# Kernel tuning notes

Measured on AMD Instinct MI355X. Metric: run time of the kernel, lower is better.

The kernel has to match this reference:

```python
import jax, jax.numpy as jnp
import numpy as np

EPS = 1e-9
TOP_K = 2


def setup_inputs() -> dict:
    key = jax.random.key(0)
    k = jax.random.split(key, 6)
    B, E, D_IN, D_MODEL, D_SEL = 16384, 8, 900, 512, 128
    return {
        "cycle_curve_data": jax.random.normal(k[0], (B, D_IN), jnp.float32),
        "logits": jax.random.normal(k[1], (B, E), jnp.float32),
        "moe_masks": jax.random.randint(k[2], (B, E), 0, 2, jnp.int32),
        "selection_embeddings": jax.random.normal(k[3], (B, E, D_SEL), jnp.float32),
        "W": jax.random.normal(k[4], (E, D_IN, D_MODEL), jnp.float32) / np.sqrt(D_IN).astype(np.float32),
        "b": jnp.zeros((E, D_MODEL), jnp.float32),
    }


def reference(cycle_curve_data, logits, moe_masks, selection_embeddings, W, b):
    B, E = logits.shape
    mask = (moe_masks == 1).astype(logits.dtype)  # [B, E]
    raw = jax.nn.softmax(logits, axis=1)          # [B, E]

    # inactive-expert mixture for selection embedding
    inactive = raw * (1.0 - mask)
    inactive = inactive / (jnp.sum(inactive, axis=1, keepdims=True) + EPS)
    selection_embedding = jnp.einsum("bes,be->bs", selection_embeddings, inactive)

    # active gates + top-k selection + renormalization
    active = raw * mask
    _, idx = jax.lax.top_k(active, TOP_K)                                  # [B, K]
    top_mask = jnp.sum(jax.nn.one_hot(idx, E, dtype=active.dtype), axis=1)  # [B, E]
    gates = active * top_mask
    gates = gates / (jnp.sum(gates, axis=1, keepdims=True) + EPS)

    # dense formulation of dispatch -> per-expert Linear -> weighted combine:
    # out[b] = sum_e gates[b,e] * (x[b] @ W[e] + b[e])
    expert_out = jnp.einsum("bd,edm->bem", cycle_curve_data, W) + b  # [B, E, D_model]
    final_out = jnp.einsum("bem,be->bm", expert_out, gates).astype(jnp.bfloat16)

    # guide loss (training-mode auxiliary loss)
    s = jnp.sum(raw * mask) / B
    guide_loss = (1.0 - s) * (1.0 - s)
    return final_out, guide_loss, selection_embedding
```

## Files before the change

kernel.cpp:

```cpp
#include <hip/hip_runtime.h>
#include <hip/hip_bf16.h>


#define B_ROWS 16384
#define DIN 900
#define DM 512
#define DSEL 128
#define KP 928
#define NKS 29
#define MAXT 192
#define EPSF 1e-9f

#define OUT_GUIDE (B_ROWS*DM)
#define OUT_SEL   (B_ROWS*DM + 1)

#define WS_COUNTS 0
#define WS_PART   512
#define WS_NT     768
#define WS_OFF    1024
#define WS_ENT    2048
#define WS_BB     9216
#define WS_PIDLR  25600
#define WS_GATEB  91136
#define WS_W8     222208
#define WS_ROWSS  746496
#define WS_WT     812032

typedef __attribute__((ext_vector_type(8))) short short8;
typedef __attribute__((ext_vector_type(8))) unsigned short ushort8;
typedef __attribute__((ext_vector_type(4))) float floatx4;

__device__ inline unsigned short f2bf(float v){
  union { __hip_bfloat16 h; unsigned short u; } c;
  c.h = __float2bfloat16(v);
  return c.u;
}
__device__ inline float bf2f(unsigned short u){
  union { unsigned int i; float f; } c;
  c.i = ((unsigned int)u) << 16;
  return c.f;
}

__global__ __launch_bounds__(256) void cvtw_k(const float* __restrict__ W,
                                              unsigned short* __restrict__ wt){
  __shared__ unsigned short tl[64][65];
  int kt = blockIdx.x, ntb = blockIdx.y, e = blockIdx.z;
  int c = threadIdx.x & 63, q = threadIdx.x >> 6;
  for (int i = 0; i < 16; i++){
    int kl = q + i*4;
    int k = kt*64 + kl;
    float v = (k < DIN) ? W[((size_t)e*DIN + k)*DM + ntb*64 + c] : 0.f;
    tl[kl][c] = f2bf(v);
  }
  __syncthreads();
  for (int i = 0; i < 16; i++){
    int nl = q + i*4;
    int k = kt*64 + c;
    if (k < KP)
      wt[((size_t)e*DM + ntb*64 + nl)*KP + k] = tl[c][nl];
  }
}

__global__ __launch_bounds__(256) void gating_k(const float* __restrict__ logits,
                                                const int* __restrict__ masks,
                                                int* __restrict__ counts,
                                                float* __restrict__ partials,
                                                int* __restrict__ pidlr,
                                                float2* __restrict__ gatesb,
                                                float* __restrict__ w8,
                                                int* __restrict__ blockbase){
  __shared__ int hist[64];
  __shared__ float wsum[4];
  int t = threadIdx.x;
  if (t < 64) hist[t] = 0;
  __syncthreads();
  int b = blockIdx.x*256 + t;
  float4 l0 = *(const float4*)&logits[(size_t)b*8];
  float4 l1 = *(const float4*)&logits[(size_t)b*8 + 4];
  int4  m0 = *(const int4*)&masks[(size_t)b*8];
  int4  m1 = *(const int4*)&masks[(size_t)b*8 + 4];
  float raw[8] = {l0.x,l0.y,l0.z,l0.w,l1.x,l1.y,l1.z,l1.w};
  int   mk[8]  = {m0.x,m0.y,m0.z,m0.w,m1.x,m1.y,m1.z,m1.w};
  float mx = raw[0];
  for (int e = 1; e < 8; e++) mx = fmaxf(mx, raw[e]);
  float Z = 0.f;
  for (int e = 0; e < 8; e++){ raw[e] = expf(raw[e]-mx); Z += raw[e]; }
  float invZ = 1.f/Z;
  float act[8], ina[8]; float srm = 0.f, isum = 0.f;
  for (int e = 0; e < 8; e++){
    raw[e] *= invZ;
    if (mk[e] == 1){ act[e] = raw[e]; ina[e] = 0.f; srm += raw[e]; }
    else           { act[e] = 0.f;    ina[e] = raw[e]; isum += raw[e]; }
  }
  float v1 = -1.f, v2 = -1.f; int e1 = 0, e2 = 0;
  for (int e = 0; e < 8; e++){
    float a = act[e];
    if (a > v1){ v2 = v1; e2 = e1; v1 = a; e1 = e; }
    else if (a > v2){ v2 = a; e2 = e; }
  }
  float den = v1 + v2 + EPSF;
  float g1 = v1/den, g2 = v2/den;
  int lo, hi; float gl, gh;
  if (e1 < e2){ lo = e1; hi = e2; gl = g1; gh = g2; }
  else        { lo = e2; hi = e1; gl = g2; gh = g1; }
  int pid = lo*8 + hi;
  float invI = 1.f/(isum + EPSF);
  for (int e = 0; e < 8; e++) w8[(size_t)b*8 + e] = ina[e]*invI;
  gatesb[b] = make_float2(gl, gh);
  int lr = atomicAdd(&hist[pid], 1);
  pidlr[b] = pid | (lr << 8);
  float s = srm;
  for (int sft = 32; sft > 0; sft >>= 1) s += __shfl_down(s, sft, 64);
  if ((t & 63) == 0) wsum[t >> 6] = s;
  __syncthreads();
  if (t < 64){
    int c = hist[t];
    int base = 0;
    if (c > 0) base = atomicAdd(&counts[t], c);
    blockbase[blockIdx.x*64 + t] = base;
  }
  if (t == 0) partials[blockIdx.x] = wsum[0] + wsum[1] + wsum[2] + wsum[3];
}

__global__ __launch_bounds__(256) void selemb_k(const float* __restrict__ sel,
                                                const float* __restrict__ w8,
                                                const int* __restrict__ pidlr,
                                                const int* __restrict__ off,
                                                const int* __restrict__ blockbase,
                                                int* __restrict__ rows_s,
                                                float* __restrict__ out){
  int t = threadIdx.x;
  int b = blockIdx.x*2 + (t >> 7);
  int d = t & 127;
  if (d == 0){
    int pl = pidlr[b];
    int p = pl & 63;
    int lr = pl >> 8;
    rows_s[off[p] + blockbase[(b >> 8)*64 + p] + lr] = b;
  }
  const float* wr = w8 + (size_t)b*8;
  const float* sb = sel + (size_t)b*(8*DSEL);
  float a = 0.f;
  for (int e = 0; e < 8; e++) a += wr[e] * sb[e*DSEL + d];
  out[OUT_SEL + (size_t)b*DSEL + d] = a;
}

__global__ void worklist_k(const int* __restrict__ counts,
                           const float* __restrict__ partials,
                           int* __restrict__ off, int* __restrict__ ntp,
                           int4* __restrict__ entries,
                           float* __restrict__ out){
  int lane = threadIdx.x;
  int c = counts[lane];
  int sc = c;
  for (int s = 1; s < 64; s <<= 1){ int v = __shfl_up(sc, s, 64); if (lane >= s) sc += v; }
  int offp = sc - c;
  off[lane] = offp;
  int nt = (c + 127) >> 7;
  int snt = nt;
  for (int s = 1; s < 64; s <<= 1){ int v = __shfl_up(snt, s, 64); if (lane >= s) snt += v; }
  int tbase = snt - nt;
  int elo = lane >> 3, ehi = lane & 7;
  for (int j = 0; j < nt; ++j){
    int nr = c - j*128; if (nr > 128) nr = 128;
    entries[tbase + j] = make_int4(elo, ehi, offp + j*128, nr);
  }
  int tot = __shfl(snt, 63, 64);
  if (lane == 0) *ntp = tot;
  float p = partials[lane];
  for (int s = 32; s > 0; s >>= 1) p += __shfl_down(p, s, 64);
  if (lane == 0){
    float sv = p * (1.f/B_ROWS);
    float d = 1.f - sv;
    out[OUT_GUIDE] = d*d;
  }
}

__global__ __launch_bounds__(256, 2) void gemm_k(const float* __restrict__ xf,
                                              const unsigned short* __restrict__ wt,
                                              const float* __restrict__ bias,
                                              const int* __restrict__ ntp,
                                              const int4* __restrict__ entries,
                                              const int* __restrict__ rows_s,
                                              const float2* __restrict__ gatesb,
                                              float* __restrict__ out){
  int tile = blockIdx.x;
  if (tile >= *ntp) return;
  int4 ent = entries[tile];
  int elo = ent.x, ehi = ent.y, start = ent.z, nrows = ent.w;

  __shared__ __align__(16) unsigned short xs[2][128*40];
  __shared__ int   gidx_s[128];
  __shared__ float glo_s[128];
  __shared__ float ghi_s[128];

  int t = threadIdx.x;
  if (t < 128){
    if (t < nrows){
      int g = rows_s[start + t];
      gidx_s[t] = g;
      float2 gg = gatesb[g];
      glo_s[t] = gg.x; ghi_s[t] = gg.y;
    } else { gidx_s[t] = -1; glo_s[t] = 0.f; ghi_s[t] = 0.f; }
  }
  __syncthreads();

  int lane = t & 63, wid = t >> 6;
  int wrow = wid >> 1, wcol = wid & 1;
  int quad = lane >> 4, l16 = lane & 15;
  int colbase = blockIdx.y*128 + wcol*64;

  int srow = t >> 1, skc = t & 1;
  int sg = gidx_s[srow];
  const float* xrow = xf + (size_t)(sg >= 0 ? sg : 0)*DIN + skc*16;

  const unsigned short* wb0 = wt + (size_t)elo*DM*KP;
  const unsigned short* wb1 = wt + (size_t)ehi*DM*KP;

  floatx4 acc[2][4][4];
  for (int i = 0; i < 2; i++) for (int j = 0; j < 4; j++) for (int k = 0; k < 4; k++)
    for (int r = 0; r < 4; r++) acc[i][j][k][r] = 0.f;

  {
    const float4* p = (const float4*)(xrow);
    float4 a0 = p[0], a1 = p[1], a2 = p[2], a3 = p[3];
    ushort8 y0, y1;
    y0[0]=f2bf(a0.x); y0[1]=f2bf(a0.y); y0[2]=f2bf(a0.z); y0[3]=f2bf(a0.w);
    y0[4]=f2bf(a1.x); y0[5]=f2bf(a1.y); y0[6]=f2bf(a1.z); y0[7]=f2bf(a1.w);
    y1[0]=f2bf(a2.x); y1[1]=f2bf(a2.y); y1[2]=f2bf(a2.z); y1[3]=f2bf(a2.w);
    y1[4]=f2bf(a3.x); y1[5]=f2bf(a3.y); y1[6]=f2bf(a3.z); y1[7]=f2bf(a3.w);
    *((ushort8*)&xs[0][srow*40 + skc*16])     = y0;
    *((ushort8*)&xs[0][srow*40 + skc*16 + 8]) = y1;
  }

  for (int ks = 0; ks < NKS; ++ks){
    __syncthreads();
    int cur = ks & 1;
    int nks = ks + 1;

    float4 b0, b1, b2, b3;
    if (nks < NKS){
      if (nks < 28){
        const float4* p = (const float4*)(xrow + nks*32);
        b0 = p[0]; b1 = p[1]; b2 = p[2]; b3 = p[3];
      } else {
        float tmp[16];
        for (int j = 0; j < 16; j++){
          int k = nks*32 + skc*16 + j;
          tmp[j] = (k < DIN) ? xrow[nks*32 + j] : 0.f;
        }
        b0 = make_float4(tmp[0],tmp[1],tmp[2],tmp[3]);
        b1 = make_float4(tmp[4],tmp[5],tmp[6],tmp[7]);
        b2 = make_float4(tmp[8],tmp[9],tmp[10],tmp[11]);
        b3 = make_float4(tmp[12],tmp[13],tmp[14],tmp[15]);
      }
    }

    short8 af[4];
    for (int mt = 0; mt < 4; ++mt)
      af[mt] = *((const short8*)&xs[cur][(wrow*64 + mt*16 + l16)*40 + quad*8]);

    for (int nt = 0; nt < 4; ++nt){
      int n = colbase + nt*16 + l16;
      short8 bf0 = *((const short8*)(wb0 + (size_t)n*KP + ks*32 + quad*8));
      short8 bf1 = *((const short8*)(wb1 + (size_t)n*KP + ks*32 + quad*8));
      for (int mt = 0; mt < 4; ++mt)
        acc[0][mt][nt] = __builtin_amdgcn_mfma_f32_16x16x32_bf16(af[mt], bf0, acc[0][mt][nt], 0, 0, 0);
      for (int mt = 0; mt < 4; ++mt)
        acc[1][mt][nt] = __builtin_amdgcn_mfma_f32_16x16x32_bf16(af[mt], bf1, acc[1][mt][nt], 0, 0, 0);
    }

    if (nks < NKS){
      ushort8 y0, y1;
      y0[0]=f2bf(b0.x); y0[1]=f2bf(b0.y); y0[2]=f2bf(b0.z); y0[3]=f2bf(b0.w);
      y0[4]=f2bf(b1.x); y0[5]=f2bf(b1.y); y0[6]=f2bf(b1.z); y0[7]=f2bf(b1.w);
      y1[0]=f2bf(b2.x); y1[1]=f2bf(b2.y); y1[2]=f2bf(b2.z); y1[3]=f2bf(b2.w);
      y1[4]=f2bf(b3.x); y1[5]=f2bf(b3.y); y1[6]=f2bf(b3.z); y1[7]=f2bf(b3.w);
      *((ushort8*)&xs[cur^1][srow*40 + skc*16])     = y0;
      *((ushort8*)&xs[cur^1][srow*40 + skc*16 + 8]) = y1;
    }
  }

  for (int nt = 0; nt < 4; ++nt){
    int n = colbase + nt*16 + l16;
    float blo = bias[elo*DM + n];
    float bhi = bias[ehi*DM + n];
    for (int mt = 0; mt < 4; ++mt){
      int rl = wrow*64 + mt*16 + quad*4;
      for (int r = 0; r < 4; ++r){
        int rr = rl + r;
        int grow = gidx_s[rr];
        if (grow >= 0){
          float v = glo_s[rr]*(acc[0][mt][nt][r] + blo) + ghi_s[rr]*(acc[1][mt][nt][r] + bhi);
          out[(size_t)grow*DM + n] = bf2f(f2bf(v));
        }
      }
    }
  }
}

extern "C" void kernel_launch(void* const* d_in, const int* in_sizes, int n_in,
                              void* d_out, int out_size, void* d_ws, size_t ws_size,
                              hipStream_t stream){
  const float* x      = (const float*)d_in[0];
  const float* logits = (const float*)d_in[1];
  const int*   masks  = (const int*)d_in[2];
  const float* sel    = (const float*)d_in[3];
  const float* W      = (const float*)d_in[4];
  const float* bias   = (const float*)d_in[5];
  float* out = (float*)d_out;
  char* ws = (char*)d_ws;
  int*    counts   = (int*)(ws + WS_COUNTS);
  float*  partials = (float*)(ws + WS_PART);
  int*    ntp      = (int*)(ws + WS_NT);
  int*    off      = (int*)(ws + WS_OFF);
  int4*   entries  = (int4*)(ws + WS_ENT);
  int*    blockbase= (int*)(ws + WS_BB);
  int*    pidlr    = (int*)(ws + WS_PIDLR);
  float2* gatesb   = (float2*)(ws + WS_GATEB);
  float*  w8       = (float*)(ws + WS_W8);
  int*    rows_s   = (int*)(ws + WS_ROWSS);
  unsigned short* wt = (unsigned short*)(ws + WS_WT);

  hipMemsetAsync(ws, 0, 256, stream);
  cvtw_k<<<dim3(15, 8, 8), 256, 0, stream>>>(W, wt);
  gating_k<<<B_ROWS/256, 256, 0, stream>>>(logits, masks, counts, partials, pidlr, gatesb, w8, blockbase);
  worklist_k<<<1, 64, 0, stream>>>(counts, partials, off, ntp, entries, out);
  selemb_k<<<B_ROWS/2, 256, 0, stream>>>(sel, w8, pidlr, off, blockbase, rows_s, out);
  gemm_k<<<dim3(MAXT, 4), 256, 0, stream>>>(x, wt, bias, ntp, entries, rows_s, gatesb, out);
}
```

Before: 340.4 us.

## Pre-swizzle weights into MFMA fragment layout and load activations directly to registers

The weight conversion kernel now writes bf16 weights in a fragment-tiled layout (16 columns by 32 k per 512-element chunk), so each lane's B fragment is one contiguous 16-byte load. The GEMM drops the LDS staging of activations and the per-step barriers. Each lane gathers its own x rows straight from global memory into registers, converts them to bf16, and software-pipelines both A and B fragments across k-steps. The cost is redundant global reads of x across waves that share rows, plus higher register pressure.

```diff
diff --git a/kernel.cpp b/kernel.cpp
--- a/kernel.cpp
+++ b/kernel.cpp
@@ -26,6 +26,8 @@
 #define WS_ROWSS  746496
 #define WS_WT     812032
 
+#define FRSTRIDE 14848
+
 typedef __attribute__((ext_vector_type(8))) short short8;
 typedef __attribute__((ext_vector_type(8))) unsigned short ushort8;
 typedef __attribute__((ext_vector_type(4))) float floatx4;
@@ -40,24 +42,38 @@
   c.i = ((unsigned int)u) << 16;
   return c.f;
 }
-
-__global__ __launch_bounds__(256) void cvtw_k(const float* __restrict__ W,
-                                              unsigned short* __restrict__ wt){
-  __shared__ unsigned short tl[64][65];
-  int kt = blockIdx.x, ntb = blockIdx.y, e = blockIdx.z;
-  int c = threadIdx.x & 63, q = threadIdx.x >> 6;
-  for (int i = 0; i < 16; i++){
-    int kl = q + i*4;
-    int k = kt*64 + kl;
-    float v = (k < DIN) ? W[((size_t)e*DIN + k)*DM + ntb*64 + c] : 0.f;
-    tl[kl][c] = f2bf(v);
+__device__ inline short8 pack8(float4 a, float4 b){
+  union { ushort8 u; short8 s; } c;
+  c.u[0]=f2bf(a.x); c.u[1]=f2bf(a.y); c.u[2]=f2bf(a.z); c.u[3]=f2bf(a.w);
+  c.u[4]=f2bf(b.x); c.u[5]=f2bf(b.y); c.u[6]=f2bf(b.z); c.u[7]=f2bf(b.w);
+  return c.s;
+}
+
+__global__ __launch_bounds__(256) void cvtw2_k(const float* __restrict__ W,
+                                               unsigned short* __restrict__ wt2){
+  __shared__ unsigned short lds[32][512];
+  int t = threadIdx.x;
+  int kc = blockIdx.x, e = blockIdx.y;
+  for (int kk = 0; kk < 32; ++kk){
+    int k = kc*32 + kk;
+    if (k < DIN){
+      const float* wr = W + ((size_t)e*DIN + k)*DM;
+      lds[kk][t]       = f2bf(wr[t]);
+      lds[kk][t + 256] = f2bf(wr[t + 256]);
+    } else {
+      lds[kk][t] = 0; lds[kk][t + 256] = 0;
+    }
   }
   __syncthreads();
-  for (int i = 0; i < 16; i++){
-    int nl = q + i*4;
-    int k = kt*64 + c;
-    if (k < KP)
-      wt[((size_t)e*DM + ntb*64 + nl)*KP + k] = tl[c][nl];
+  int ncg = t >> 3, q = t & 7;
+  unsigned short* ob = wt2 + (((size_t)e*32 + ncg)*29 + kc)*512;
+  for (int i = 0; i < 8; ++i){
+    int fb = i*64 + q*8;
+    int col = fb >> 5, kk0 = fb & 31;
+    ushort8 y;
+    #pragma unroll
+    for (int j = 0; j < 8; ++j) y[j] = lds[kk0 + j][ncg*16 + col];
+    *((ushort8*)(ob + fb)) = y;
   }
 }
 
@@ -176,123 +192,138 @@
   }
 }
 
+
+#define LDRAW(kks) { \
+  r0 = *(const float4*)(ap0 + (kks)*32); r1 = *(const float4*)(ap0 + (kks)*32 + 4); \
+  r2 = *(const float4*)(ap1 + (kks)*32); r3 = *(const float4*)(ap1 + (kks)*32 + 4); \
+  r4 = *(const float4*)(ap2 + (kks)*32); r5 = *(const float4*)(ap2 + (kks)*32 + 4); \
+  r6 = *(const float4*)(ap3 + (kks)*32); r7 = *(const float4*)(ap3 + (kks)*32 + 4); }
+
+#define LDRAW_TAIL() { \
+  float4 z = make_float4(0.f,0.f,0.f,0.f); \
+  float4 t0 = *(const float4*)(ap0 - quad*8 + 896); \
+  float4 t1 = *(const float4*)(ap1 - quad*8 + 896); \
+  float4 t2 = *(const float4*)(ap2 - quad*8 + 896); \
+  float4 t3 = *(const float4*)(ap3 - quad*8 + 896); \
+  r0 = (quad==0)? t0 : z; r1 = z; \
+  r2 = (quad==0)? t1 : z; r3 = z; \
+  r4 = (quad==0)? t2 : z; r5 = z; \
+  r6 = (quad==0)? t3 : z; r7 = z; }
+
+#define CVT(dst) { \
+  dst##0 = pack8(r0, r1); dst##1 = pack8(r2, r3); \
+  dst##2 = pack8(r4, r5); dst##3 = pack8(r6, r7); }
+
+#define MF(afX, b, ei, nt) { \
+  acc[ei][0][nt] = __builtin_amdgcn_mfma_f32_16x16x32_bf16(afX##0, b, acc[ei][0][nt], 0, 0, 0); \
+  acc[ei][1][nt] = __builtin_amdgcn_mfma_f32_16x16x32_bf16(afX##1, b, acc[ei][1][nt], 0, 0, 0); \
+  acc[ei][2][nt] = __builtin_amdgcn_mfma_f32_16x16x32_bf16(afX##2, b, acc[ei][2][nt], 0, 0, 0); \
+  acc[ei][3][nt] = __builtin_amdgcn_mfma_f32_16x16x32_bf16(afX##3, b, acc[ei][3][nt], 0, 0, 0); }
+
+#define STEP(afX, kks, LASTF) { \
+  short8 b0n, b1n; \
+   \
+  b0n = *((const short8*)(bp0 + 1*FRSTRIDE + (kks)*512)); \
+  b1n = *((const short8*)(bp1 + 1*FRSTRIDE + (kks)*512)); \
+  MF(afX, b0c, 0, 0); MF(afX, b1c, 1, 0); b0c = b0n; b1c = b1n; \
+   \
+  b0n = *((const short8*)(bp0 + 2*FRSTRIDE + (kks)*512)); \
+  b1n = *((const short8*)(bp1 + 2*FRSTRIDE + (kks)*512)); \
+  MF(afX, b0c, 0, 1); MF(afX, b1c, 1, 1); b0c = b0n; b1c = b1n; \
+   \
+  b0n = *((const short8*)(bp0 + 3*FRSTRIDE + (kks)*512)); \
+  b1n = *((const short8*)(bp1 + 3*FRSTRIDE + (kks)*512)); \
+  MF(afX, b0c, 0, 2); MF(afX, b1c, 1, 2); b0c = b0n; b1c = b1n; \
+   \
+  if (!(LASTF)){ \
+    b0n = *((const short8*)(bp0 + ((kks)+1)*512)); \
+    b1n = *((const short8*)(bp1 + ((kks)+1)*512)); \
+  } \
+  MF(afX, b0c, 0, 3); MF(afX, b1c, 1, 3); b0c = b0n; b1c = b1n; }
+
 __global__ __launch_bounds__(256, 2) void gemm_k(const float* __restrict__ xf,
-                                              const unsigned short* __restrict__ wt,
-                                              const float* __restrict__ bias,
-                                              const int* __restrict__ ntp,
-                                              const int4* __restrict__ entries,
-                                              const int* __restrict__ rows_s,
-                                              const float2* __restrict__ gatesb,
-                                              float* __restrict__ out){
+                                                 const unsigned short* __restrict__ wt2,
+                                                 const float* __restrict__ bias,
+                                                 const int* __restrict__ ntp,
+                                                 const int4* __restrict__ entries,
+                                                 const int* __restrict__ rows_s,
+                                                 const float2* __restrict__ gatesb,
+                                                 float* __restrict__ out){
   int tile = blockIdx.x;
   if (tile >= *ntp) return;
   int4 ent = entries[tile];
   int elo = ent.x, ehi = ent.y, start = ent.z, nrows = ent.w;
 
-  __shared__ __align__(16) unsigned short xs[2][128*40];
-  __shared__ int   gidx_s[128];
-  __shared__ float glo_s[128];
-  __shared__ float ghi_s[128];
-
-  int t = threadIdx.x;
-  if (t < 128){
-    if (t < nrows){
-      int g = rows_s[start + t];
-      gidx_s[t] = g;
-      float2 gg = gatesb[g];
-      glo_s[t] = gg.x; ghi_s[t] = gg.y;
-    } else { gidx_s[t] = -1; glo_s[t] = 0.f; ghi_s[t] = 0.f; }
-  }
-  __syncthreads();
-
-  int lane = t & 63, wid = t >> 6;
+  int t = threadIdx.x, lane = t & 63, wid = t >> 6;
   int wrow = wid >> 1, wcol = wid & 1;
   int quad = lane >> 4, l16 = lane & 15;
-  int colbase = blockIdx.y*128 + wcol*64;
-
-  int srow = t >> 1, skc = t & 1;
-  int sg = gidx_s[srow];
-  const float* xrow = xf + (size_t)(sg >= 0 ? sg : 0)*DIN + skc*16;
-
-  const unsigned short* wb0 = wt + (size_t)elo*DM*KP;
-  const unsigned short* wb1 = wt + (size_t)ehi*DM*KP;
+  int ncg0 = blockIdx.y*8 + wcol*4;
+
+  const float* ap0; const float* ap1; const float* ap2; const float* ap3;
+  {
+    int rr, g;
+    rr = wrow*64 + 0*16 + l16; g = (rr < nrows) ? rows_s[start + rr] : 0;
+    ap0 = xf + (size_t)g*DIN + quad*8;
+    rr = wrow*64 + 1*16 + l16; g = (rr < nrows) ? rows_s[start + rr] : 0;
+    ap1 = xf + (size_t)g*DIN + quad*8;
+    rr = wrow*64 + 2*16 + l16; g = (rr < nrows) ? rows_s[start + rr] : 0;
+    ap2 = xf + (size_t)g*DIN + quad*8;
+    rr = wrow*64 + 3*16 + l16; g = (rr < nrows) ? rows_s[start + rr] : 0;
+    ap3 = xf + (size_t)g*DIN + quad*8;
+  }
+  const unsigned short* bp0 = wt2 + ((size_t)(elo*32 + ncg0)*29)*512 + l16*32 + quad*8;
+  const unsigned short* bp1 = wt2 + ((size_t)(ehi*32 + ncg0)*29)*512 + l16*32 + quad*8;
 
   floatx4 acc[2][4][4];
-  for (int i = 0; i < 2; i++) for (int j = 0; j < 4; j++) for (int k = 0; k < 4; k++)
-    for (int r = 0; r < 4; r++) acc[i][j][k][r] = 0.f;
-
-  {
-    const float4* p = (const float4*)(xrow);
-    float4 a0 = p[0], a1 = p[1], a2 = p[2], a3 = p[3];
-    ushort8 y0, y1;
-    y0[0]=f2bf(a0.x); y0[1]=f2bf(a0.y); y0[2]=f2bf(a0.z); y0[3]=f2bf(a0.w);
-    y0[4]=f2bf(a1.x); y0[5]=f2bf(a1.y); y0[6]=f2bf(a1.z); y0[7]=f2bf(a1.w);
-    y1[0]=f2bf(a2.x); y1[1]=f2bf(a2.y); y1[2]=f2bf(a2.z); y1[3]=f2bf(a2.w);
-    y1[4]=f2bf(a3.x); y1[5]=f2bf(a3.y); y1[6]=f2bf(a3.z); y1[7]=f2bf(a3.w);
-    *((ushort8*)&xs[0][srow*40 + skc*16])     = y0;
-    *((ushort8*)&xs[0][srow*40 + skc*16 + 8]) = y1;
-  }
-
-  for (int ks = 0; ks < NKS; ++ks){
-    __syncthreads();
-    int cur = ks & 1;
-    int nks = ks + 1;
-
-    float4 b0, b1, b2, b3;
-    if (nks < NKS){
-      if (nks < 28){
-        const float4* p = (const float4*)(xrow + nks*32);
-        b0 = p[0]; b1 = p[1]; b2 = p[2]; b3 = p[3];
-      } else {
-        float tmp[16];
-        for (int j = 0; j < 16; j++){
-          int k = nks*32 + skc*16 + j;
-          tmp[j] = (k < DIN) ? xrow[nks*32 + j] : 0.f;
-        }
-        b0 = make_float4(tmp[0],tmp[1],tmp[2],tmp[3]);
-        b1 = make_float4(tmp[4],tmp[5],tmp[6],tmp[7]);
-        b2 = make_float4(tmp[8],tmp[9],tmp[10],tmp[11]);
-        b3 = make_float4(tmp[12],tmp[13],tmp[14],tmp[15]);
-      }
-    }
-
-    short8 af[4];
-    for (int mt = 0; mt < 4; ++mt)
-      af[mt] = *((const short8*)&xs[cur][(wrow*64 + mt*16 + l16)*40 + quad*8]);
-
-    for (int nt = 0; nt < 4; ++nt){
-      int n = colbase + nt*16 + l16;
-      short8 bf0 = *((const short8*)(wb0 + (size_t)n*KP + ks*32 + quad*8));
-      short8 bf1 = *((const short8*)(wb1 + (size_t)n*KP + ks*32 + quad*8));
-      for (int mt = 0; mt < 4; ++mt)
-        acc[0][mt][nt] = __builtin_amdgcn_mfma_f32_16x16x32_bf16(af[mt], bf0, acc[0][mt][nt], 0, 0, 0);
-      for (int mt = 0; mt < 4; ++mt)
-        acc[1][mt][nt] = __builtin_amdgcn_mfma_f32_16x16x32_bf16(af[mt], bf1, acc[1][mt][nt], 0, 0, 0);
-    }
-
-    if (nks < NKS){
-      ushort8 y0, y1;
-      y0[0]=f2bf(b0.x); y0[1]=f2bf(b0.y); y0[2]=f2bf(b0.z); y0[3]=f2bf(b0.w);
-      y0[4]=f2bf(b1.x); y0[5]=f2bf(b1.y); y0[6]=f2bf(b1.z); y0[7]=f2bf(b1.w);
-      y1[0]=f2bf(b2.x); y1[1]=f2bf(b2.y); y1[2]=f2bf(b2.z); y1[3]=f2bf(b2.w);
-      y1[4]=f2bf(b3.x); y1[5]=f2bf(b3.y); y1[6]=f2bf(b3.z); y1[7]=f2bf(b3.w);
-      *((ushort8*)&xs[cur^1][srow*40 + skc*16])     = y0;
-      *((ushort8*)&xs[cur^1][srow*40 + skc*16 + 8]) = y1;
-    }
-  }
-
+  #pragma unroll
+  for (int i = 0; i < 2; i++)
+    #pragma unroll
+    for (int j = 0; j < 4; j++)
+      #pragma unroll
+      for (int k = 0; k < 4; k++)
+        #pragma unroll
+        for (int r = 0; r < 4; r++) acc[i][j][k][r] = 0.f;
+
+  float4 r0,r1,r2,r3,r4,r5,r6,r7;
+  short8 afA0, afA1, afA2, afA3;
+  short8 afB0, afB1, afB2, afB3;
+
+  LDRAW(0);
+  CVT(afA);
+  short8 b0c = *((const short8*)(bp0));
+  short8 b1c = *((const short8*)(bp1));
+
+  for (int ks = 0; ks < 28; ks += 2){
+    LDRAW(ks+1);
+    STEP(afA, ks, false);
+    CVT(afB);
+    if (ks + 2 < 28){ LDRAW(ks+2); } else { LDRAW_TAIL(); }
+    STEP(afB, ks+1, false);
+    CVT(afA);
+  }
+  STEP(afA, 28, true);
+
+  float blo[4], bhi[4];
+  #pragma unroll
   for (int nt = 0; nt < 4; ++nt){
-    int n = colbase + nt*16 + l16;
-    float blo = bias[elo*DM + n];
-    float bhi = bias[ehi*DM + n];
-    for (int mt = 0; mt < 4; ++mt){
-      int rl = wrow*64 + mt*16 + quad*4;
-      for (int r = 0; r < 4; ++r){
-        int rr = rl + r;
-        int grow = gidx_s[rr];
-        if (grow >= 0){
-          float v = glo_s[rr]*(acc[0][mt][nt][r] + blo) + ghi_s[rr]*(acc[1][mt][nt][r] + bhi);
-          out[(size_t)grow*DM + n] = bf2f(f2bf(v));
+    int n = (ncg0 + nt)*16 + l16;
+    blo[nt] = bias[elo*DM + n];
+    bhi[nt] = bias[ehi*DM + n];
+  }
+  #pragma unroll
+  for (int mt = 0; mt < 4; ++mt){
+    #pragma unroll
+    for (int r = 0; r < 4; ++r){
+      int rr = wrow*64 + mt*16 + quad*4 + r;
+      if (rr < nrows){
+        int grow = rows_s[start + rr];
+        float2 gg = gatesb[grow];
+        float* orow = out + (size_t)grow*DM;
+        #pragma unroll
+        for (int nt = 0; nt < 4; ++nt){
+          int n = (ncg0 + nt)*16 + l16;
+          float v = gg.x*(acc[0][mt][nt][r] + blo[nt]) + gg.y*(acc[1][mt][nt][r] + bhi[nt]);
+          orow[n] = bf2f(f2bf(v));
         }
       }
     }
@@ -320,12 +351,12 @@
   float2* gatesb   = (float2*)(ws + WS_GATEB);
   float*  w8       = (float*)(ws + WS_W8);
   int*    rows_s   = (int*)(ws + WS_ROWSS);
-  unsigned short* wt = (unsigned short*)(ws + WS_WT);
+  unsigned short* wt2 = (unsigned short*)(ws + WS_WT);
 
   hipMemsetAsync(ws, 0, 256, stream);
-  cvtw_k<<<dim3(15, 8, 8), 256, 0, stream>>>(W, wt);
+  cvtw2_k<<<dim3(29, 8), 256, 0, stream>>>(W, wt2);
   gating_k<<<B_ROWS/256, 256, 0, stream>>>(logits, masks, counts, partials, pidlr, gatesb, w8, blockbase);
   worklist_k<<<1, 64, 0, stream>>>(counts, partials, off, ntp, entries, out);
   selemb_k<<<B_ROWS/2, 256, 0, stream>>>(sel, w8, pidlr, off, blockbase, rows_s, out);
-  gemm_k<<<dim3(MAXT, 4), 256, 0, stream>>>(x, wt, bias, ntp, entries, rows_s, gatesb, out);
-}
+  gemm_k<<<dim3(MAXT, 4), 256, 0, stream>>>(x, wt2, bias, ntp, entries, rows_s, gatesb, out);
+}
```

After: 332.6 us. 2.3% less time.
